# Performance work log

Hardware: AMD Instinct MI355X
Metric: run time of the kernel (lower is better)

The kernel has to match this reference:

```python
import jax, jax.numpy as jnp
import numpy as np
from jax import lax

NF = 64; LAT = 512; IMG = 64; NC = 4
DILS = (1, 2, 4, 8)                 # dilated 3x3 sobel: effective kernels 3,5,9,17 w/ pads 1,2,4,8
CF = 1 + 2 * len(DILS)              # identity + (sobel_x, sobel_y) per scale -> 9
FIN = NF * CF; FH = NF; FO = NF     # DynaResidualBlock dims
NFREQ = 6; FCH = 4 * NFREQ          # sin/cos over x and y per frequency -> 24 pos channels
CAT = LAT + NF * FCH                # input dim of out_to_lat blocks (512 + 1536 = 2048)
P_DYN = FH * FIN + FH + FO * FH + FO + FO * FIN + FO


def _make_pe():
    c = (np.arange(IMG, dtype=np.float32) + 0.5) / IMG
    yy, xx = np.meshgrid(c, c, indexing='ij')
    ch = []
    for u in (xx, yy):
        for f in range(NFREQ):
            w = (2.0 ** f) * 2.0 * np.pi
            ch.append(np.sin(w * u)); ch.append(np.cos(w * u))
    return jnp.asarray(np.stack(ch, 0).astype(np.float32))   # [FCH, H, W]


def _lin_res(x, w1, b1, w2, b2, ws, bs):
    # LinearResidualBlock: skip linear + 2-layer MLP with LeakyReLU(0.2)
    return x @ ws + bs + jax.nn.leaky_relu(x @ w1 + b1, 0.2) @ w2 + b2

_SX = jnp.array([[-1., 0., 1.], [-2., 0., 2.], [-1., 0., 1.]], jnp.float32) / 8.0
_SY = _SX.T


def _perceive(x):
    # multi-scale sobel perception (RandGrads): identity + depthwise dilated sobel x/y
    feats = [x]
    dn = ('NCHW', 'OIHW', 'NCHW')
    for d in DILS:
        for k in (_SX, _SY):
            kern = jnp.broadcast_to(k, (NF, 1, 3, 3))
            feats.append(lax.conv_general_dilated(
                x, kern, (1, 1), [(d, d), (d, d)],
                rhs_dilation=(d, d), dimension_numbers=dn,
                feature_group_count=NF))
    return jnp.concatenate(feats, axis=1)   # [B, NF*CF, H, W]


def _inorm(x, eps=1e-5):
    # InstanceNorm2d (affine=False)
    m = x.mean((2, 3), keepdims=True)
    v = ((x - m) ** 2).mean((2, 3), keepdims=True)
    return (x - m) * lax.rsqrt(v + eps)


def _dyna_conv(x, lat, dyn_w, dyn_b):
    # DynaResidualBlock: hypernetwork generates per-sample 1x1 conv weights from lat
    B = x.shape[0]
    p = lat @ dyn_w + dyn_b                 # [B, P_DYN]
    o = 0
    def take(n):
        nonlocal o
        q = p[:, o:o + n]; o += n; return q
    k_in = take(FH * FIN).reshape(B, FH, FIN); b_in = take(FH)
    k_out = take(FO * FH).reshape(B, FO, FH); b_out = take(FO)
    k_sk = take(FO * FIN).reshape(B, FO, FIN); b_sk = take(FO)
    h = jnp.einsum('bfi,bihw->bfhw', k_in, x) + b_in[:, :, None, None]
    h = jax.nn.leaky_relu(h, 0.2)
    y = jnp.einsum('bof,bfhw->bohw', k_out, h) + b_out[:, :, None, None]
    s = jnp.einsum('boi,bihw->bohw', k_sk, x) + b_sk[:, :, None, None]
    return s + y


def setup_inputs() -> dict:
    key = jax.random.key(0)
    ks = jax.random.split(key, 16)
    g = lambda i, shape, s=0.02: jax.random.normal(ks[i], shape, jnp.float32) * s
    z = lambda shape: jnp.zeros(shape, jnp.float32)
    return {
        'x': jax.random.normal(ks[0], (16, 3, IMG, IMG), jnp.float32),
        'inj_lat': jax.random.normal(ks[1], (16, LAT), jnp.float32),
        'w_in': g(2, (NF, 3), 0.3), 'b_in': z((NF,)),
        'fl_w1': g(3, (LAT, LAT)), 'fl_b1': z((LAT,)),
        'fl_w2': g(4, (LAT, LAT)), 'fl_b2': z((LAT,)),
        'fl_ws': g(5, (LAT, LAT)), 'fl_bs': z((LAT,)),
        'dyn_w': g(6, (LAT, P_DYN), 0.002), 'dyn_b': g(7, (P_DYN,), 0.002),
        'pe': _make_pe(),
        'otl_w1': g(8, (NC, CAT, CAT)), 'otl_b1': z((NC, CAT)),
        'otl_w2': g(9, (NC, CAT, LAT)), 'otl_b2': z((NC, LAT)),
        'otl_ws': g(10, (NC, CAT, LAT)), 'otl_bs': z((NC, LAT)),
        'ltl_w': g(11, (LAT, LAT)), 'ltl_b': z((LAT,)),
    }


def reference(x, inj_lat, w_in, b_in, fl_w1, fl_b1, fl_w2, fl_b2, fl_ws, fl_bs,
              dyn_w, dyn_b, pe, otl_w1, otl_b1, otl_w2, otl_b2, otl_ws, otl_bs,
              ltl_w, ltl_b):
    B = x.shape[0]
    out = jnp.einsum('oc,bchw->bohw', w_in, x) + b_in[None, :, None, None]  # in_conv (1x1)
    lat = jnp.zeros((B, LAT), x.dtype)
    for c in range(NC):
        inj_lat = _lin_res(inj_lat, fl_w1, fl_b1, fl_w2, fl_b2, fl_ws, fl_bs)
        out = _dyna_conv(_inorm(_perceive(out)), inj_lat, dyn_w, dyn_b)
        # ConvFreqEncoding(out).mean((2,3)) == contraction of out with pos encodings
        freq = jnp.einsum('bchw,fhw->bcf', out, pe).reshape(B, -1) / (IMG * IMG)
        lat = _lin_res(jnp.concatenate([lat, freq], axis=1),
                       otl_w1[c], otl_b1[c], otl_w2[c], otl_b2[c], otl_ws[c], otl_bs[c])
    return lat @ ltl_w + ltl_b
```

## Files before the change

### kernel.cpp

```cpp
#include <hip/hip_runtime.h>
#include <hip/hip_bf16.h>
#include <cstdint>
#include <cstddef>

#define PIX   4096
#define PDYN  78016
#define LATD  512
#define CATD  2048

typedef unsigned short u16;
typedef __attribute__((ext_vector_type(8))) short bf16x8;
typedef __attribute__((ext_vector_type(4))) float f32x4;
#define MFMA16(a,b,c) __builtin_amdgcn_mfma_f32_16x16x32_bf16(a,b,c,0,0,0)

__device__ __forceinline__ float lrelu(float v) { return v > 0.f ? v : 0.2f * v; }
__device__ __forceinline__ unsigned bfbits(float x) {
  __hip_bfloat16 h = __float2bfloat16(x);
  return (unsigned)*(unsigned short*)&h;
}
__device__ __forceinline__ unsigned pack2(float a, float b) {
  return bfbits(a) | (bfbits(b) << 16);
}

__global__ void k_zero(float* __restrict__ p, int n) {
  int i = blockIdx.x * 256 + threadIdx.x;
  if (i < n) p[i] = 0.f;
}

__global__ void k_init_out(const float* __restrict__ x, const float* __restrict__ w_in,
                           const float* __restrict__ b_in, float* __restrict__ out) {
  int idx = blockIdx.x * 256 + threadIdx.x;
  int p = idx & 4095, o = (idx >> 12) & 63, b = idx >> 18;
  const float* xb = x + (size_t)b * 3 * PIX + p;
  out[idx] = b_in[o] + w_in[o*3+0]*xb[0] + w_in[o*3+1]*xb[PIX] + w_in[o*3+2]*xb[2*PIX];
}

__global__ void k_cat_init(const float* __restrict__ lat, float* __restrict__ cat) {
  int idx = blockIdx.x * 256 + threadIdx.x;
  int j = idx & 2047, b = idx >> 11;
  cat[idx] = (j < 512) ? lat[b*512 + j] : 0.f;
}

__global__ void k_pe(const float* __restrict__ pe, u16* __restrict__ peB) {
  int idx = blockIdx.x * 256 + threadIdx.x;
  int j = idx & 7, lane = (idx >> 3) & 63, kc = (idx >> 9) & 3, ft = (idx >> 11) & 1, pt = idx >> 12;
  int f = ft*16 + (lane & 15);
  int p = pt*128 + kc*32 + (lane >> 4)*8 + j;
  peB[idx] = (f < 24) ? (u16)bfbits(pe[(size_t)f*PIX + p]) : (u16)0;
}

__device__ __forceinline__ void feat9(const float (*ch)[65], int h, int w, float* f) {
  f[0] = ch[h][w];
#pragma unroll
  for (int di = 0; di < 4; ++di) {
    int d = 1 << di;
    bool hm = (h - d) >= 0, hp = (h + d) < 64;
    bool wm = (w - d) >= 0, wp = (w + d) < 64;
    float tm = (hm && wm) ? ch[h-d][w-d] : 0.f;
    float t0 =  hm        ? ch[h-d][w  ] : 0.f;
    float tp = (hm && wp) ? ch[h-d][w+d] : 0.f;
    float mm =  wm        ? ch[h  ][w-d] : 0.f;
    float mp =  wp        ? ch[h  ][w+d] : 0.f;
    float bm = (hp && wm) ? ch[h+d][w-d] : 0.f;
    float b0 =  hp        ? ch[h+d][w  ] : 0.f;
    float bp = (hp && wp) ? ch[h+d][w+d] : 0.f;
    f[1 + 2*di] = (tp - tm + 2.f*(mp - mm) + bp - bm) * 0.125f;
    f[2 + 2*di] = (bm - tm + 2.f*(b0 - t0) + bp - tp) * 0.125f;
  }
}

__global__ __launch_bounds__(256) void k_prep(const float* __restrict__ out,
                                              __hip_bfloat16* __restrict__ xn) {
  __shared__ float ch[64][65];
  __shared__ float redS[4][9], redQ[4][9];
  __shared__ float mS[9], rS[9];
  int c = blockIdx.x, b = blockIdx.y, t = threadIdx.x;
  const float* src = out + ((size_t)b * 64 + c) * PIX;
  for (int j = 0; j < 16; ++j) { int idx = t + j*256; ch[idx >> 6][idx & 63] = src[idx]; }
  __syncthreads();
  float s[9], q[9];
#pragma unroll
  for (int k = 0; k < 9; ++k) { s[k] = 0.f; q[k] = 0.f; }
  for (int j = 0; j < 16; ++j) {
    int p = t + j*256; int h = p >> 6, w = p & 63;
    float f[9]; feat9(ch, h, w, f);
#pragma unroll
    for (int k = 0; k < 9; ++k) { s[k] += f[k]; q[k] += f[k]*f[k]; }
  }
#pragma unroll
  for (int off = 32; off; off >>= 1)
#pragma unroll
    for (int k = 0; k < 9; ++k) { s[k] += __shfl_down(s[k], off, 64); q[k] += __shfl_down(q[k], off, 64); }
  int lane = t & 63, wv = t >> 6;
  if (lane == 0)
#pragma unroll
    for (int k = 0; k < 9; ++k) { redS[wv][k] = s[k]; redQ[wv][k] = q[k]; }
  __syncthreads();
  if (t < 9) {
    float ss = 0.f, qq = 0.f;
    for (int w2 = 0; w2 < 4; ++w2) { ss += redS[w2][t]; qq += redQ[w2][t]; }
    float mean = ss * (1.f/4096.f);
    float var  = qq * (1.f/4096.f) - mean*mean;
    mS[t] = mean; rS[t] = rsqrtf(var + 1e-5f);
  }
  __syncthreads();
  for (int j = 0; j < 16; ++j) {
    int p = t + j*256; int h = p >> 6, w = p & 63;
    float f[9]; feat9(ch, h, w, f);
#pragma unroll
    for (int k = 0; k < 9; ++k)
      xn[((size_t)b * 576 + k*64 + c) * PIX + p] = __float2bfloat16((f[k] - mS[k]) * rS[k]);
  }
}

__global__ void k_fold(const float* __restrict__ P, u16* __restrict__ Wst, int cyc) {
  int idx = blockIdx.x * 256 + threadIdx.x;
  int b = blockIdx.y;
  int kk = idx & 31, m = (idx >> 5) & 127, kg = idx >> 12;
  int f = kg*32 + kk;
  const float* row = P + (size_t)(cyc*16 + b) * PDYN;
  float v = (m < 64) ? row[m*576 + f] : row[41088 + (m-64)*576 + f];
  Wst[(size_t)b * 73728 + idx] = (u16)bfbits(v);
}

__global__ void k_koutfold(const float* __restrict__ P, u16* __restrict__ KoutF, int cyc) {
  int idx = blockIdx.x * 256 + threadIdx.x;
  int j = idx & 7, lane = (idx >> 3) & 63, kc = (idx >> 9) & 1, ot = (idx >> 10) & 3, b = idx >> 12;
  int o = ot*16 + (lane & 15);
  int m = kc*32 + (lane >> 4)*8 + j;
  KoutF[idx] = (u16)bfbits(P[(size_t)(cyc*16 + b) * PDYN + 36928 + o*64 + m]);
}

__global__ void k_biascopy(const float* __restrict__ P, float* __restrict__ biasf, int cyc) {
  int idx = blockIdx.x * 256 + threadIdx.x;
  int b = idx >> 7, m = idx & 127;
  const float* row = P + (size_t)(cyc*16 + b) * PDYN;
  biasf[idx] = (m < 64) ? row[36864 + m] : (row[77952 + (m-64)] + row[41024 + (m-64)]);
}

__global__ __launch_bounds__(256) void k_dyna(
    const u16* __restrict__ Wst, const u16* __restrict__ xn,
    const u16* __restrict__ KoutF, const u16* __restrict__ peB,
    const float* __restrict__ biasf, float* __restrict__ out,
    float* __restrict__ cat) {
  __shared__ u16 lds[16384];
  u16* As = lds;
  u16* Xl = lds + 8192;

  int t = threadIdx.x;
  int lane = t & 63, wv = t >> 6;
  int col = lane & 15, quad = lane >> 4;
  int b = blockIdx.y, p0 = blockIdx.x * 128;

  const u16* WB  = Wst + (size_t)b * 73728;
  const u16* xnB = xn  + (size_t)b * 576 * PIX + p0;

  f32x4 acc[8][2];
#pragma unroll
  for (int i = 0; i < 8; ++i) { acc[i][0] = {0.f,0.f,0.f,0.f}; acc[i][1] = {0.f,0.f,0.f,0.f}; }

  int sm = t & 127, skg = t >> 7, s7 = sm & 7;
  int pg = t & 15, kq = t >> 4;

  for (int kb = 0; kb < 9; ++kb) {
    uint4 w[4];
    const uint4* wsrc = (const uint4*)(WB + (size_t)kb*8192 + sm*32 + skg*4096);
    wsrc = (const uint4*)(WB + (size_t)kb*8192 + t*32);
#pragma unroll
    for (int q = 0; q < 4; ++q) w[q] = wsrc[q];
    uint4 xr[4];
#pragma unroll
    for (int kk = 0; kk < 4; ++kk)
      xr[kk] = *(const uint4*)(xnB + (size_t)(kb*64 + kq*4 + kk)*PIX + pg*8);
    __syncthreads();
#pragma unroll
    for (int q = 0; q < 4; ++q)
      *(uint4*)&As[sm*64 + (((skg*4 + q) ^ s7) * 8)] = w[q];
    const unsigned* xw = (const unsigned*)xr;
    unsigned pkl[8], pkh[8];
#pragma unroll
    for (int i = 0; i < 8; ++i) {
      unsigned sh = (i & 1) * 16;
      unsigned h0 = (xw[0  + (i>>1)] >> sh) & 0xffffu;
      unsigned h1 = (xw[4  + (i>>1)] >> sh) & 0xffffu;
      unsigned h2 = (xw[8  + (i>>1)] >> sh) & 0xffffu;
      unsigned h3 = (xw[12 + (i>>1)] >> sh) & 0xffffu;
      pkl[i] = h0 | (h1 << 16);
      pkh[i] = h2 | (h3 << 16);
    }
    int ch0 = kq >> 1, sub = (kq & 1) * 4;
#pragma unroll
    for (int jj = 0; jj < 8; ++jj) {
      int i = (jj + pg) & 7;
      int p = pg*8 + i;
      *(uint2*)&Xl[p*64 + ((ch0 ^ i) * 8) + sub] = make_uint2(pkl[i], pkh[i]);
    }
    __syncthreads();
#pragma unroll
    for (int kc = 0; kc < 2; ++kc) {
      bf16x8 bfr[2];
#pragma unroll
      for (int nt = 0; nt < 2; ++nt) {
        int n = wv*32 + nt*16 + col;
        bfr[nt] = *(const bf16x8*)&Xl[n*64 + (((kc*4 + quad) ^ (n & 7)) * 8)];
      }
#pragma unroll
      for (int mt = 0; mt < 8; ++mt) {
        int m = mt*16 + col;
        bf16x8 af = *(const bf16x8*)&As[m*64 + (((kc*4 + quad) ^ (m & 7)) * 8)];
        acc[mt][0] = MFMA16(af, bfr[0], acc[mt][0]);
        acc[mt][1] = MFMA16(af, bfr[1], acc[mt][1]);
      }
    }
  }
  __syncthreads();

  const float* bfB = biasf + b*128;
#pragma unroll
  for (int mt = 0; mt < 4; ++mt) {
    float bm[4];
#pragma unroll
    for (int r = 0; r < 4; ++r) bm[r] = bfB[mt*16 + quad*4 + r];
#pragma unroll
    for (int nt = 0; nt < 2; ++nt) {
      unsigned lo = pack2(lrelu(acc[mt][nt][0] + bm[0]), lrelu(acc[mt][nt][1] + bm[1]));
      unsigned hi = pack2(lrelu(acc[mt][nt][2] + bm[2]), lrelu(acc[mt][nt][3] + bm[3]));
      int nl = nt*16 + col;
      int ch = (mt*2 + (quad >> 1)) ^ (nl & 7);
      *(uint2*)&As[(wv*32 + nl)*64 + ch*8 + (quad & 1)*4] = make_uint2(lo, hi);
    }
  }
  __syncthreads();

  f32x4 yac[4][2];
#pragma unroll
  for (int i = 0; i < 4; ++i) { yac[i][0] = {0.f,0.f,0.f,0.f}; yac[i][1] = {0.f,0.f,0.f,0.f}; }
  const u16* kofB = KoutF + (size_t)b * 4096;
#pragma unroll
  for (int kc = 0; kc < 2; ++kc) {
    bf16x8 hb[2];
#pragma unroll
    for (int nt = 0; nt < 2; ++nt) {
      int nl = nt*16 + col;
      hb[nt] = *(const bf16x8*)&As[(wv*32 + nl)*64 + (((kc*4 + quad) ^ (nl & 7)) * 8)];
    }
#pragma unroll
    for (int ot = 0; ot < 4; ++ot) {
      bf16x8 ka = *(const bf16x8*)&kofB[((ot*2 + kc)*64 + lane) * 8];
      yac[ot][0] = MFMA16(ka, hb[0], yac[ot][0]);
      yac[ot][1] = MFMA16(ka, hb[1], yac[ot][1]);
    }
  }
#pragma unroll
  for (int ot = 0; ot < 4; ++ot) {
    float bo[4];
#pragma unroll
    for (int r = 0; r < 4; ++r) bo[r] = bfB[64 + ot*16 + quad*4 + r];
#pragma unroll
    for (int nt = 0; nt < 2; ++nt) {
      int pl = wv*32 + nt*16 + col;
#pragma unroll
      for (int r = 0; r < 4; ++r) {
        float rs = acc[4 + ot][nt][r] + yac[ot][nt][r] + bo[r];
        int o = ot*16 + quad*4 + r;
        out[((size_t)b*64 + o)*PIX + p0 + pl] = rs;
        Xl[o*128 + (((pl >> 3) ^ (o & 7)) * 8) + (pl & 7)] = (u16)bfbits(rs);
      }
    }
  }
  __syncthreads();

  f32x4 fac[4][2];
#pragma unroll
  for (int i = 0; i < 4; ++i) { fac[i][0] = {0.f,0.f,0.f,0.f}; fac[i][1] = {0.f,0.f,0.f,0.f}; }
  bf16x8 pb[2];
#pragma unroll
  for (int ft = 0; ft < 2; ++ft)
    pb[ft] = *(const bf16x8*)&peB[((((size_t)blockIdx.x*2 + ft)*4 + wv)*64 + lane) * 8];
#pragma unroll
  for (int mt = 0; mt < 4; ++mt) {
    int o = mt*16 + col;
    bf16x8 ar = *(const bf16x8*)&Xl[o*128 + (((wv*4 + quad) ^ (o & 7)) * 8)];
    fac[mt][0] = MFMA16(ar, pb[0], fac[mt][0]);
    fac[mt][1] = MFMA16(ar, pb[1], fac[mt][1]);
  }
  __syncthreads();
  float* fred = (float*)lds;
#pragma unroll
  for (int mt = 0; mt < 4; ++mt)
#pragma unroll
    for (int ft = 0; ft < 2; ++ft)
#pragma unroll
      for (int r = 0; r < 4; ++r)
        fred[(wv*64 + mt*16 + quad*4 + r)*32 + ft*16 + col] = fac[mt][ft][r];
  __syncthreads();
  for (int pr = t; pr < 1536; pr += 256) {
    int o = pr / 24, f = pr - o*24;
    float s = fred[o*32 + f] + fred[(64 + o)*32 + f] + fred[(128 + o)*32 + f] + fred[(192 + o)*32 + f];
    atomicAdd(&cat[b*CATD + 512 + o*24 + f], s * (1.f/4096.f));
  }
}

__global__ __launch_bounds__(256) void gemm_wide(
    const float* __restrict__ A, const float* __restrict__ Bm,
    float* __restrict__ C, const float* __restrict__ bias, int M, int N, int K) {
  __shared__ float As[16][68];
  __shared__ float Bs[16][64];
  int t = threadIdx.x;
  int tx = t & 15, ty = t >> 4;
  int m0 = blockIdx.y * 64, n0 = blockIdx.x * 64;
  float acc[4][4];
#pragma unroll
  for (int i = 0; i < 4; ++i)
#pragma unroll
    for (int j = 0; j < 4; ++j) acc[i][j] = 0.f;
  for (int k0 = 0; k0 < K; k0 += 16) {
#pragma unroll
    for (int j = 0; j < 4; ++j) {
      int r = (t >> 4) + j*16, c = t & 15;
      As[c][r] = (m0 + r < M) ? A[(size_t)(m0 + r)*K + k0 + c] : 0.f;
    }
#pragma unroll
    for (int j = 0; j < 4; ++j) {
      int idx = t + j*256;
      int kr = idx >> 6, nc = idx & 63;
      Bs[kr][nc] = Bm[(size_t)(k0 + kr)*N + n0 + nc];
    }
    __syncthreads();
#pragma unroll
    for (int kk = 0; kk < 16; ++kk) {
      float4 av = *(const float4*)&As[kk][ty*4];
      float4 bv = *(const float4*)&Bs[kk][tx*4];
      float a[4] = {av.x, av.y, av.z, av.w};
      float bb[4] = {bv.x, bv.y, bv.z, bv.w};
#pragma unroll
      for (int i = 0; i < 4; ++i)
#pragma unroll
        for (int j = 0; j < 4; ++j) acc[i][j] += a[i]*bb[j];
    }
    __syncthreads();
  }
#pragma unroll
  for (int i = 0; i < 4; ++i) {
    int rowg = m0 + ty*4 + i;
    if (rowg < M)
#pragma unroll
      for (int j = 0; j < 4; ++j) {
        int col = n0 + tx*4 + j;
        C[(size_t)rowg*N + col] = acc[i][j] + bias[col];
      }
  }
}

__global__ __launch_bounds__(256) void gemm_skinny(
    const float* __restrict__ A, const float* __restrict__ Bm,
    float* __restrict__ C, const float* __restrict__ bias,
    int N, int K, int act, int accum) {
  __shared__ float As[16][17];
  __shared__ float Bs[16][64];
  int t = threadIdx.x;
  int row = t & 15, cg = t >> 4;
  int n0 = blockIdx.x * 64;
  int ks = gridDim.y;
  int kchunk = K / ks;
  int k0base = blockIdx.y * kchunk;
  float acc[4] = {0.f, 0.f, 0.f, 0.f};
  for (int k0 = k0base; k0 < k0base + kchunk; k0 += 16) {
    { int lr = t >> 4, lc = t & 15; As[lc][lr] = A[(size_t)lr*K + k0 + lc]; }
#pragma unroll
    for (int j = 0; j < 4; ++j) {
      int idx = t + j*256;
      int kr = idx >> 6, nc = idx & 63;
      Bs[kr][nc] = Bm[(size_t)(k0 + kr)*N + n0 + nc];
    }
    __syncthreads();
#pragma unroll
    for (int kk = 0; kk < 16; ++kk) {
      float a = As[kk][row];
      float4 bv = *(const float4*)&Bs[kk][cg*4];
      acc[0] += a*bv.x; acc[1] += a*bv.y; acc[2] += a*bv.z; acc[3] += a*bv.w;
    }
    __syncthreads();
  }
  if (ks > 1) {
    float* Pp = C + (size_t)blockIdx.y * 16 * N;
#pragma unroll
    for (int j = 0; j < 4; ++j) Pp[(size_t)row*N + n0 + cg*4 + j] = acc[j];
  } else {
#pragma unroll
    for (int j = 0; j < 4; ++j) {
      int col = n0 + cg*4 + j;
      float v = acc[j] + bias[col];
      if (accum) v += C[(size_t)row*N + col];
      if (act) v = lrelu(v);
      C[(size_t)row*N + col] = v;
    }
  }
}

__global__ void k_reduce(float* __restrict__ C,
                         const float* __restrict__ P1, int ns1, const float* __restrict__ bias1,
                         const float* __restrict__ P2, int ns2, const float* __restrict__ bias2,
                         int nmask, int total, int act, int accum) {
  int idx = blockIdx.x * 256 + threadIdx.x;
  if (idx >= total) return;
  int col = idx & nmask;
  float v = bias1[col];
  for (int s = 0; s < ns1; ++s) v += P1[(size_t)s*total + idx];
  if (P2) { v += bias2[col]; for (int s = 0; s < ns2; ++s) v += P2[(size_t)s*total + idx]; }
  if (act) v = lrelu(v);
  if (accum) v += C[idx];
  C[idx] = v;
}

extern "C" void kernel_launch(void* const* d_in, const int* in_sizes, int n_in,
                              void* d_out, int out_size, void* d_ws, size_t ws_size,
                              hipStream_t stream) {
  const float* x      = (const float*)d_in[0];
  const float* inj0   = (const float*)d_in[1];
  const float* w_in   = (const float*)d_in[2];
  const float* b_in   = (const float*)d_in[3];
  const float* fl_w1  = (const float*)d_in[4];
  const float* fl_b1  = (const float*)d_in[5];
  const float* fl_w2  = (const float*)d_in[6];
  const float* fl_b2  = (const float*)d_in[7];
  const float* fl_ws  = (const float*)d_in[8];
  const float* fl_bs  = (const float*)d_in[9];
  const float* dyn_w  = (const float*)d_in[10];
  const float* dyn_b  = (const float*)d_in[11];
  const float* pe     = (const float*)d_in[12];
  const float* otl_w1 = (const float*)d_in[13];
  const float* otl_b1 = (const float*)d_in[14];
  const float* otl_w2 = (const float*)d_in[15];
  const float* otl_b2 = (const float*)d_in[16];
  const float* otl_ws = (const float*)d_in[17];
  const float* otl_bs = (const float*)d_in[18];
  const float* ltl_w  = (const float*)d_in[19];
  const float* ltl_b  = (const float*)d_in[20];
  float* outF = (float*)d_out;

  char* w = (char*)d_ws;
  float* inj_seq = (float*)(w + 0);
  float* tmpA    = (float*)(w + 131072);
  float* lat     = (float*)(w + 262144);
  float* cat     = (float*)(w + 294912);
  float* biasf   = (float*)(w + 425984);
  float* part1   = (float*)(w + 434176);
  float* part2   = (float*)(w + 2531328);
  float* part3   = (float*)(w + 2793472);
  u16*   Wst     = (u16*)  (w + 3055616);
  u16*   KoutF   = (u16*)  (w + 5414912);
  u16*   peB     = (u16*)  (w + 5545984);
  float* Pbuf    = (float*)(w + 5808128);
  float* outb    = (float*)(w + 25780224);
  u16*   xnb     = (u16*)  (w + 42557440);

  k_zero<<<32, 256, 0, stream>>>(lat, 16*512);
  k_init_out<<<16384, 256, 0, stream>>>(x, w_in, b_in, outb);
  k_pe<<<512, 256, 0, stream>>>(pe, peB);

  for (int c = 0; c < 4; ++c) {
    const float* src = (c == 0) ? inj0 : (inj_seq + (size_t)(c-1)*16*LATD);
    float* dst = inj_seq + (size_t)c*16*LATD;
    gemm_skinny<<<dim3(8,8), 256, 0, stream>>>(src,  fl_w1, part2, nullptr, 512, 512, 0, 0);
    k_reduce<<<32, 256, 0, stream>>>(tmpA, part2, 8, fl_b1, nullptr, 0, nullptr, 511, 8192, 1, 0);
    gemm_skinny<<<dim3(8,8), 256, 0, stream>>>(src,  fl_ws, part3, nullptr, 512, 512, 0, 0);
    k_reduce<<<32, 256, 0, stream>>>(dst, part3, 8, fl_bs, nullptr, 0, nullptr, 511, 8192, 0, 0);
    gemm_skinny<<<dim3(8,8), 256, 0, stream>>>(tmpA, fl_w2, part2, nullptr, 512, 512, 0, 0);
    k_reduce<<<32, 256, 0, stream>>>(dst, part2, 8, fl_b2, nullptr, 0, nullptr, 511, 8192, 0, 1);
  }
  gemm_wide<<<dim3(PDYN/64, 1), 256, 0, stream>>>(inj_seq, dyn_w, Pbuf, dyn_b, 64, PDYN, 512);

  for (int c = 0; c < 4; ++c) {
    k_prep<<<dim3(64,16), 256, 0, stream>>>(outb, (__hip_bfloat16*)xnb);
    k_fold<<<dim3(288,16), 256, 0, stream>>>(Pbuf, Wst, c);
    k_koutfold<<<256, 256, 0, stream>>>(Pbuf, KoutF, c);
    k_biascopy<<<8, 256, 0, stream>>>(Pbuf, biasf, c);
    k_cat_init<<<128, 256, 0, stream>>>(lat, cat);
    k_dyna<<<dim3(32,16), 256, 0, stream>>>(Wst, xnb, KoutF, peB, biasf, outb, cat);
    gemm_skinny<<<dim3(32,16), 256, 0, stream>>>(cat, otl_w1 + (size_t)c*CATD*CATD, part1, nullptr, 2048, 2048, 0, 0);
    k_reduce<<<128, 256, 0, stream>>>(tmpA, part1, 16, otl_b1 + c*CATD,
                                      nullptr, 0, nullptr, 2047, 16*2048, 1, 0);
    gemm_skinny<<<dim3(8,8), 256, 0, stream>>>(cat,  otl_ws + (size_t)c*CATD*LATD, part2, nullptr, 512, 2048, 0, 0);
    gemm_skinny<<<dim3(8,8), 256, 0, stream>>>(tmpA, otl_w2 + (size_t)c*CATD*LATD, part3, nullptr, 512, 2048, 0, 0);
    k_reduce<<<32, 256, 0, stream>>>(lat, part2, 8, otl_bs + c*LATD,
                                     part3, 8, otl_b2 + c*LATD, 511, 16*512, 0, 0);
  }
  gemm_skinny<<<dim3(8,8), 256, 0, stream>>>(lat, ltl_w, part2, nullptr, 512, 512, 0, 0);
  k_reduce<<<32, 256, 0, stream>>>(outF, part2, 8, ltl_b, nullptr, 0, nullptr, 511, 8192, 0, 0);
}
```

Before: 1.033 ms.

## Replace hypernetwork fp32 GEMM with bf16 MFMA GEMM writing folded layouts directly

The large hypernetwork GEMM (64 x 78016 x 512) moves from an FP32 scalar tiled kernel to a bf16 MFMA kernel. Its epilogue scatters results straight into the per-cycle folded weight, kout and bias layouts that k_dyna reads, which removes the Pbuf intermediate and the per-cycle fold, koutfold and biascopy kernels. Sibling skinny GEMMs that share an input (w1/ws) are merged into a single launch, the reductions are combined, and the K-split for the otl_w2 GEMM is increased. Rounding the hypernetwork inputs and weights to bf16 lowers accuracy, and the epilogue writes are scattered rather than coalesced.

```diff
diff --git a/kernel.cpp b/kernel.cpp
--- a/kernel.cpp
+++ b/kernel.cpp
@@ -47,6 +47,14 @@
   int f = ft*16 + (lane & 15);
   int p = pt*128 + kc*32 + (lane >> 4)*8 + j;
   peB[idx] = (f < 24) ? (u16)bfbits(pe[(size_t)f*PIX + p]) : (u16)0;
+}
+
+__global__ void k_afold(const float* __restrict__ inj_seq, u16* __restrict__ Abf) {
+  int idx = blockIdx.x * 256 + threadIdx.x;
+  int j = idx & 7, lane = (idx >> 3) & 63, mt = (idx >> 9) & 3, kc = (idx >> 11) & 1, kb = idx >> 12;
+  int m = mt*16 + (lane & 15);
+  int k = kb*64 + kc*32 + (lane >> 4)*8 + j;
+  Abf[idx] = (u16)bfbits(inj_seq[m*512 + k]);
 }
 
 __device__ __forceinline__ void feat9(const float (*ch)[65], int h, int w, float* f) {
@@ -113,36 +121,99 @@
   }
 }
 
-__global__ void k_fold(const float* __restrict__ P, u16* __restrict__ Wst, int cyc) {
-  int idx = blockIdx.x * 256 + threadIdx.x;
-  int b = blockIdx.y;
-  int kk = idx & 31, m = (idx >> 5) & 127, kg = idx >> 12;
-  int f = kg*32 + kk;
-  const float* row = P + (size_t)(cyc*16 + b) * PDYN;
-  float v = (m < 64) ? row[m*576 + f] : row[41088 + (m-64)*576 + f];
-  Wst[(size_t)b * 73728 + idx] = (u16)bfbits(v);
-}
-
-__global__ void k_koutfold(const float* __restrict__ P, u16* __restrict__ KoutF, int cyc) {
-  int idx = blockIdx.x * 256 + threadIdx.x;
-  int j = idx & 7, lane = (idx >> 3) & 63, kc = (idx >> 9) & 1, ot = (idx >> 10) & 3, b = idx >> 12;
-  int o = ot*16 + (lane & 15);
-  int m = kc*32 + (lane >> 4)*8 + j;
-  KoutF[idx] = (u16)bfbits(P[(size_t)(cyc*16 + b) * PDYN + 36928 + o*64 + m]);
-}
-
-__global__ void k_biascopy(const float* __restrict__ P, float* __restrict__ biasf, int cyc) {
-  int idx = blockIdx.x * 256 + threadIdx.x;
-  int b = idx >> 7, m = idx & 127;
-  const float* row = P + (size_t)(cyc*16 + b) * PDYN;
-  biasf[idx] = (m < 64) ? row[36864 + m] : (row[77952 + (m-64)] + row[41024 + (m-64)]);
+__global__ __launch_bounds__(256) void k_pgemm(
+    const u16* __restrict__ Abf, const float* __restrict__ Bw,
+    const float* __restrict__ bias, u16* __restrict__ Wst4,
+    u16* __restrict__ KoutF4, float* __restrict__ biasf4) {
+  __shared__ u16 Xl[128 * 64];
+  int t = threadIdx.x;
+  int lane = t & 63, wv = t >> 6;
+  int col = lane & 15, quad = lane >> 4;
+  int n0 = blockIdx.x * 128;
+  int pg = t & 15, kq = t >> 4;
+
+  f32x4 acc[4][2];
+#pragma unroll
+  for (int i = 0; i < 4; ++i) { acc[i][0] = {0.f,0.f,0.f,0.f}; acc[i][1] = {0.f,0.f,0.f,0.f}; }
+
+  bool vld = (n0 + pg*8) < PDYN;
+
+  for (int kb = 0; kb < 8; ++kb) {
+    float br[4][8];
+#pragma unroll
+    for (int kk = 0; kk < 4; ++kk) {
+      const float* src = Bw + (size_t)(kb*64 + kq*4 + kk)*PDYN + n0 + pg*8;
+      float4 a0 = vld ? *(const float4*)src       : float4{0.f,0.f,0.f,0.f};
+      float4 a1 = vld ? *(const float4*)(src + 4) : float4{0.f,0.f,0.f,0.f};
+      br[kk][0]=a0.x; br[kk][1]=a0.y; br[kk][2]=a0.z; br[kk][3]=a0.w;
+      br[kk][4]=a1.x; br[kk][5]=a1.y; br[kk][6]=a1.z; br[kk][7]=a1.w;
+    }
+    __syncthreads();
+    int ch0 = kq >> 1, sub = (kq & 1) * 4;
+#pragma unroll
+    for (int jj = 0; jj < 8; ++jj) {
+      int i = (jj + pg) & 7;
+      unsigned lo = pack2(br[0][i], br[1][i]);
+      unsigned hi = pack2(br[2][i], br[3][i]);
+      int p = pg*8 + i;
+      *(uint2*)&Xl[p*64 + ((ch0 ^ i) * 8) + sub] = make_uint2(lo, hi);
+    }
+    __syncthreads();
+#pragma unroll
+    for (int kc = 0; kc < 2; ++kc) {
+      bf16x8 bfr[2];
+#pragma unroll
+      for (int nt = 0; nt < 2; ++nt) {
+        int n = wv*32 + nt*16 + col;
+        bfr[nt] = *(const bf16x8*)&Xl[n*64 + (((kc*4 + quad) ^ (n & 7)) * 8)];
+      }
+#pragma unroll
+      for (int mt = 0; mt < 4; ++mt) {
+        bf16x8 af = *(const bf16x8*)&Abf[(((kb*2 + kc)*4 + mt)*64 + lane) * 8];
+        acc[mt][0] = MFMA16(af, bfr[0], acc[mt][0]);
+        acc[mt][1] = MFMA16(af, bfr[1], acc[mt][1]);
+      }
+    }
+  }
+
+#pragma unroll
+  for (int nt = 0; nt < 2; ++nt) {
+    int pcol = n0 + wv*32 + nt*16 + col;
+    if (pcol >= PDYN) continue;
+    float bb = bias[pcol];
+#pragma unroll
+    for (int mt = 0; mt < 4; ++mt) {
+#pragma unroll
+      for (int r = 0; r < 4; ++r) {
+        int lb = mt*16 + quad*4 + r;
+        float v = acc[mt][nt][r] + bb;
+        if (pcol < 36864) {
+          int o = pcol / 576, f = pcol - o*576;
+          Wst4[(size_t)lb*73728 + (f>>5)*4096 + o*32 + (f&31)] = (u16)bfbits(v);
+        } else if (pcol < 36928) {
+          biasf4[lb*192 + (pcol - 36864)] = v;
+        } else if (pcol < 41024) {
+          int q = pcol - 36928; int o = q >> 6, m = q & 63;
+          int lk = ((m & 31) >> 3)*16 + (o & 15);
+          KoutF4[(size_t)lb*4096 + (((o>>4)*2 + (m>>5))*64 + lk)*8 + (m & 7)] = (u16)bfbits(v);
+        } else if (pcol < 41088) {
+          biasf4[lb*192 + 64 + (pcol - 41024)] = v;
+        } else if (pcol < 77952) {
+          int q = pcol - 41088; int o = q / 576, f = q - o*576;
+          Wst4[(size_t)lb*73728 + (f>>5)*4096 + (64 + o)*32 + (f&31)] = (u16)bfbits(v);
+        } else {
+          biasf4[lb*192 + 128 + (pcol - 77952)] = v;
+        }
+      }
+    }
+  }
 }
 
 __global__ __launch_bounds__(256) void k_dyna(
-    const u16* __restrict__ Wst, const u16* __restrict__ xn,
-    const u16* __restrict__ KoutF, const u16* __restrict__ peB,
-    const float* __restrict__ biasf, float* __restrict__ out,
-    float* __restrict__ cat) {
+    const u16* __restrict__ Wst4, const u16* __restrict__ xn,
+    const u16* __restrict__ KoutF4, const u16* __restrict__ peB,
+    const float* __restrict__ biasf4, float* __restrict__ out,
+    float* __restrict__ cat, int cyc) {
   __shared__ u16 lds[16384];
   u16* As = lds;
   u16* Xl = lds + 8192;
@@ -152,7 +223,7 @@
   int col = lane & 15, quad = lane >> 4;
   int b = blockIdx.y, p0 = blockIdx.x * 128;
 
-  const u16* WB  = Wst + (size_t)b * 73728;
+  const u16* WB  = Wst4 + (size_t)(cyc*16 + b) * 73728;
   const u16* xnB = xn  + (size_t)b * 576 * PIX + p0;
 
   f32x4 acc[8][2];
@@ -161,11 +232,11 @@
 
   int sm = t & 127, skg = t >> 7, s7 = sm & 7;
   int pg = t & 15, kq = t >> 4;
+  (void)skg; (void)sm; (void)s7;
 
   for (int kb = 0; kb < 9; ++kb) {
     uint4 w[4];
-    const uint4* wsrc = (const uint4*)(WB + (size_t)kb*8192 + sm*32 + skg*4096);
-    wsrc = (const uint4*)(WB + (size_t)kb*8192 + t*32);
+    const uint4* wsrc = (const uint4*)(WB + (size_t)kb*8192 + t*32);
 #pragma unroll
     for (int q = 0; q < 4; ++q) w[q] = wsrc[q];
     uint4 xr[4];
@@ -173,9 +244,12 @@
     for (int kk = 0; kk < 4; ++kk)
       xr[kk] = *(const uint4*)(xnB + (size_t)(kb*64 + kq*4 + kk)*PIX + pg*8);
     __syncthreads();
-#pragma unroll
-    for (int q = 0; q < 4; ++q)
-      *(uint4*)&As[sm*64 + (((skg*4 + q) ^ s7) * 8)] = w[q];
+    {
+      int m = t & 127, kg = t >> 7, m7 = m & 7;
+#pragma unroll
+      for (int q = 0; q < 4; ++q)
+        *(uint4*)&As[m*64 + (((kg*4 + q) ^ m7) * 8)] = w[q];
+    }
     const unsigned* xw = (const unsigned*)xr;
     unsigned pkl[8], pkh[8];
 #pragma unroll
@@ -215,7 +289,7 @@
   }
   __syncthreads();
 
-  const float* bfB = biasf + b*128;
+  const float* bfB = biasf4 + (size_t)(cyc*16 + b) * 192;
 #pragma unroll
   for (int mt = 0; mt < 4; ++mt) {
     float bm[4];
@@ -235,7 +309,7 @@
   f32x4 yac[4][2];
 #pragma unroll
   for (int i = 0; i < 4; ++i) { yac[i][0] = {0.f,0.f,0.f,0.f}; yac[i][1] = {0.f,0.f,0.f,0.f}; }
-  const u16* kofB = KoutF + (size_t)b * 4096;
+  const u16* kofB = KoutF4 + (size_t)(cyc*16 + b) * 4096;
 #pragma unroll
   for (int kc = 0; kc < 2; ++kc) {
     bf16x8 hb[2];
@@ -255,7 +329,10 @@
   for (int ot = 0; ot < 4; ++ot) {
     float bo[4];
 #pragma unroll
-    for (int r = 0; r < 4; ++r) bo[r] = bfB[64 + ot*16 + quad*4 + r];
+    for (int r = 0; r < 4; ++r) {
+      int o = ot*16 + quad*4 + r;
+      bo[r] = bfB[64 + o] + bfB[128 + o];
+    }
 #pragma unroll
     for (int nt = 0; nt < 2; ++nt) {
       int pl = wv*32 + nt*16 + col;
@@ -301,61 +378,9 @@
   }
 }
 
-__global__ __launch_bounds__(256) void gemm_wide(
-    const float* __restrict__ A, const float* __restrict__ Bm,
-    float* __restrict__ C, const float* __restrict__ bias, int M, int N, int K) {
-  __shared__ float As[16][68];
-  __shared__ float Bs[16][64];
-  int t = threadIdx.x;
-  int tx = t & 15, ty = t >> 4;
-  int m0 = blockIdx.y * 64, n0 = blockIdx.x * 64;
-  float acc[4][4];
-#pragma unroll
-  for (int i = 0; i < 4; ++i)
-#pragma unroll
-    for (int j = 0; j < 4; ++j) acc[i][j] = 0.f;
-  for (int k0 = 0; k0 < K; k0 += 16) {
-#pragma unroll
-    for (int j = 0; j < 4; ++j) {
-      int r = (t >> 4) + j*16, c = t & 15;
-      As[c][r] = (m0 + r < M) ? A[(size_t)(m0 + r)*K + k0 + c] : 0.f;
-    }
-#pragma unroll
-    for (int j = 0; j < 4; ++j) {
-      int idx = t + j*256;
-      int kr = idx >> 6, nc = idx & 63;
-      Bs[kr][nc] = Bm[(size_t)(k0 + kr)*N + n0 + nc];
-    }
-    __syncthreads();
-#pragma unroll
-    for (int kk = 0; kk < 16; ++kk) {
-      float4 av = *(const float4*)&As[kk][ty*4];
-      float4 bv = *(const float4*)&Bs[kk][tx*4];
-      float a[4] = {av.x, av.y, av.z, av.w};
-      float bb[4] = {bv.x, bv.y, bv.z, bv.w};
-#pragma unroll
-      for (int i = 0; i < 4; ++i)
-#pragma unroll
-        for (int j = 0; j < 4; ++j) acc[i][j] += a[i]*bb[j];
-    }
-    __syncthreads();
-  }
-#pragma unroll
-  for (int i = 0; i < 4; ++i) {
-    int rowg = m0 + ty*4 + i;
-    if (rowg < M)
-#pragma unroll
-      for (int j = 0; j < 4; ++j) {
-        int col = n0 + tx*4 + j;
-        C[(size_t)rowg*N + col] = acc[i][j] + bias[col];
-      }
-  }
-}
-
 __global__ __launch_bounds__(256) void gemm_skinny(
     const float* __restrict__ A, const float* __restrict__ Bm,
-    float* __restrict__ C, const float* __restrict__ bias,
-    int N, int K, int act, int accum) {
+    float* __restrict__ C, int N, int K) {
   __shared__ float As[16][17];
   __shared__ float Bs[16][64];
   int t = threadIdx.x;
@@ -382,20 +407,47 @@
     }
     __syncthreads();
   }
-  if (ks > 1) {
-    float* Pp = C + (size_t)blockIdx.y * 16 * N;
-#pragma unroll
-    for (int j = 0; j < 4; ++j) Pp[(size_t)row*N + n0 + cg*4 + j] = acc[j];
-  } else {
+  float* Pp = C + (size_t)blockIdx.y * 16 * N;
+#pragma unroll
+  for (int j = 0; j < 4; ++j) Pp[(size_t)row*N + n0 + cg*4 + j] = acc[j];
+}
+
+__global__ __launch_bounds__(256) void gemm_skinny2(
+    const float* __restrict__ A,
+    const float* __restrict__ B1, float* __restrict__ C1, int N1, int tiles1,
+    const float* __restrict__ B2, float* __restrict__ C2, int N2, int K) {
+  __shared__ float As[16][17];
+  __shared__ float Bs[16][64];
+  int bx = blockIdx.x;
+  const float* Bm; float* C; int N, n0;
+  if (bx < tiles1) { Bm = B1; C = C1; N = N1; n0 = bx*64; }
+  else             { Bm = B2; C = C2; N = N2; n0 = (bx - tiles1)*64; }
+  int t = threadIdx.x;
+  int row = t & 15, cg = t >> 4;
+  int ks = gridDim.y;
+  int kchunk = K / ks;
+  int k0base = blockIdx.y * kchunk;
+  float acc[4] = {0.f, 0.f, 0.f, 0.f};
+  for (int k0 = k0base; k0 < k0base + kchunk; k0 += 16) {
+    { int lr = t >> 4, lc = t & 15; As[lc][lr] = A[(size_t)lr*K + k0 + lc]; }
 #pragma unroll
     for (int j = 0; j < 4; ++j) {
-      int col = n0 + cg*4 + j;
-      float v = acc[j] + bias[col];
-      if (accum) v += C[(size_t)row*N + col];
-      if (act) v = lrelu(v);
-      C[(size_t)row*N + col] = v;
-    }
-  }
+      int idx = t + j*256;
+      int kr = idx >> 6, nc = idx & 63;
+      Bs[kr][nc] = Bm[(size_t)(k0 + kr)*N + n0 + nc];
+    }
+    __syncthreads();
+#pragma unroll
+    for (int kk = 0; kk < 16; ++kk) {
+      float a = As[kk][row];
+      float4 bv = *(const float4*)&Bs[kk][cg*4];
+      acc[0] += a*bv.x; acc[1] += a*bv.y; acc[2] += a*bv.z; acc[3] += a*bv.w;
+    }
+    __syncthreads();
+  }
+  float* Pp = C + (size_t)blockIdx.y * 16 * N;
+#pragma unroll
+  for (int j = 0; j < 4; ++j) Pp[(size_t)row*N + n0 + cg*4 + j] = acc[j];
 }
 
 __global__ void k_reduce(float* __restrict__ C,
@@ -444,16 +496,16 @@
   float* tmpA    = (float*)(w + 131072);
   float* lat     = (float*)(w + 262144);
   float* cat     = (float*)(w + 294912);
-  float* biasf   = (float*)(w + 425984);
-  float* part1   = (float*)(w + 434176);
-  float* part2   = (float*)(w + 2531328);
-  float* part3   = (float*)(w + 2793472);
-  u16*   Wst     = (u16*)  (w + 3055616);
-  u16*   KoutF   = (u16*)  (w + 5414912);
-  u16*   peB     = (u16*)  (w + 5545984);
-  float* Pbuf    = (float*)(w + 5808128);
-  float* outb    = (float*)(w + 25780224);
-  u16*   xnb     = (u16*)  (w + 42557440);
+  float* biasf4  = (float*)(w + 425984);
+  float* part1   = (float*)(w + 475136);
+  float* part2   = (float*)(w + 2572288);
+  float* part3   = (float*)(w + 3096576);
+  u16*   Wst4    = (u16*)  (w + 3620864);
+  u16*   KoutF4  = (u16*)  (w + 13058048);
+  u16*   Abf     = (u16*)  (w + 13582336);
+  u16*   peB     = (u16*)  (w + 13647872);
+  float* outb    = (float*)(w + 13910016);
+  u16*   xnb     = (u16*)  (w + 30687232);
 
   k_zero<<<32, 256, 0, stream>>>(lat, 16*512);
   k_init_out<<<16384, 256, 0, stream>>>(x, w_in, b_in, outb);
@@ -462,30 +514,26 @@
   for (int c = 0; c < 4; ++c) {
     const float* src = (c == 0) ? inj0 : (inj_seq + (size_t)(c-1)*16*LATD);
     float* dst = inj_seq + (size_t)c*16*LATD;
-    gemm_skinny<<<dim3(8,8), 256, 0, stream>>>(src,  fl_w1, part2, nullptr, 512, 512, 0, 0);
+    gemm_skinny2<<<dim3(16,8), 256, 0, stream>>>(src, fl_w1, part2, 512, 8, fl_ws, part3, 512, 512);
     k_reduce<<<32, 256, 0, stream>>>(tmpA, part2, 8, fl_b1, nullptr, 0, nullptr, 511, 8192, 1, 0);
-    gemm_skinny<<<dim3(8,8), 256, 0, stream>>>(src,  fl_ws, part3, nullptr, 512, 512, 0, 0);
-    k_reduce<<<32, 256, 0, stream>>>(dst, part3, 8, fl_bs, nullptr, 0, nullptr, 511, 8192, 0, 0);
-    gemm_skinny<<<dim3(8,8), 256, 0, stream>>>(tmpA, fl_w2, part2, nullptr, 512, 512, 0, 0);
-    k_reduce<<<32, 256, 0, stream>>>(dst, part2, 8, fl_b2, nullptr, 0, nullptr, 511, 8192, 0, 1);
-  }
-  gemm_wide<<<dim3(PDYN/64, 1), 256, 0, stream>>>(inj_seq, dyn_w, Pbuf, dyn_b, 64, PDYN, 512);
+    gemm_skinny<<<dim3(8,8), 256, 0, stream>>>(tmpA, fl_w2, part2, 512, 512);
+    k_reduce<<<32, 256, 0, stream>>>(dst, part3, 8, fl_bs, part2, 8, fl_b2, 511, 8192, 0, 0);
+  }
+  k_afold<<<128, 256, 0, stream>>>(inj_seq, Abf);
+  k_pgemm<<<610, 256, 0, stream>>>(Abf, dyn_w, dyn_b, Wst4, KoutF4, biasf4);
 
   for (int c = 0; c < 4; ++c) {
     k_prep<<<dim3(64,16), 256, 0, stream>>>(outb, (__hip_bfloat16*)xnb);
-    k_fold<<<dim3(288,16), 256, 0, stream>>>(Pbuf, Wst, c);
-    k_koutfold<<<256, 256, 0, stream>>>(Pbuf, KoutF, c);
-    k_biascopy<<<8, 256, 0, stream>>>(Pbuf, biasf, c);
     k_cat_init<<<128, 256, 0, stream>>>(lat, cat);
-    k_dyna<<<dim3(32,16), 256, 0, stream>>>(Wst, xnb, KoutF, peB, biasf, outb, cat);
-    gemm_skinny<<<dim3(32,16), 256, 0, stream>>>(cat, otl_w1 + (size_t)c*CATD*CATD, part1, nullptr, 2048, 2048, 0, 0);
+    k_dyna<<<dim3(32,16), 256, 0, stream>>>(Wst4, xnb, KoutF4, peB, biasf4, outb, cat, c);
+    gemm_skinny2<<<dim3(40,16), 256, 0, stream>>>(cat, otl_w1 + (size_t)c*CATD*CATD, part1, 2048, 32,
+                                                  otl_ws + (size_t)c*CATD*LATD, part3, 512, 2048);
     k_reduce<<<128, 256, 0, stream>>>(tmpA, part1, 16, otl_b1 + c*CATD,
                                       nullptr, 0, nullptr, 2047, 16*2048, 1, 0);
-    gemm_skinny<<<dim3(8,8), 256, 0, stream>>>(cat,  otl_ws + (size_t)c*CATD*LATD, part2, nullptr, 512, 2048, 0, 0);
-    gemm_skinny<<<dim3(8,8), 256, 0, stream>>>(tmpA, otl_w2 + (size_t)c*CATD*LATD, part3, nullptr, 512, 2048, 0, 0);
-    k_reduce<<<32, 256, 0, stream>>>(lat, part2, 8, otl_bs + c*LATD,
-                                     part3, 8, otl_b2 + c*LATD, 511, 16*512, 0, 0);
-  }
-  gemm_skinny<<<dim3(8,8), 256, 0, stream>>>(lat, ltl_w, part2, nullptr, 512, 512, 0, 0);
+    gemm_skinny<<<dim3(8,16), 256, 0, stream>>>(tmpA, otl_w2 + (size_t)c*CATD*LATD, part2, 512, 2048);
+    k_reduce<<<32, 256, 0, stream>>>(lat, part3, 16, otl_bs + c*LATD,
+                                     part2, 16, otl_b2 + c*LATD, 511, 16*512, 0, 0);
+  }
+  gemm_skinny<<<dim3(8,8), 256, 0, stream>>>(lat, ltl_w, part2, 512, 512);
   k_reduce<<<32, 256, 0, stream>>>(outF, part2, 8, ltl_b, nullptr, 0, nullptr, 511, 8192, 0, 0);
 }
```

Result: faster. 916.8 us (-11.2%).
